# Performance work log

Measured on AMD Instinct MI355X. Metric: run time of the kernel, lower is better.

The kernel has to match this reference:

```python
import jax, jax.numpy as jnp
import numpy as np

TOP_K = 2          # n_activated_experts
ROUTE_SCALE = 1.0  # args.route_scale


def setup_inputs() -> dict:
    key = jax.random.key(0)
    ks = jax.random.split(key, 12)
    B, S, D, I, E = 8, 2048, 512, 1024, 8
    SH = 2 * I  # n_shared_experts * moe_inter_dim
    std = 0.02
    return {
        "x": jax.random.normal(ks[0], (B, S, D), jnp.float32),
        "gate_w": (jax.random.normal(ks[1], (E, D), jnp.float32) * std),
        "w1": (jax.random.normal(ks[2], (E, D, I), jnp.float32) * std),
        "w2": (jax.random.normal(ks[3], (E, I, D), jnp.float32) * std),
        "w3": (jax.random.normal(ks[4], (E, D, I), jnp.float32) * std),
        "sw1": (jax.random.normal(ks[5], (D, SH), jnp.float32) * std),
        "sb1": jnp.zeros((SH,), jnp.float32),
        "sw2": (jax.random.normal(ks[6], (SH, D), jnp.float32) * std),
        "sb2": jnp.zeros((D,), jnp.float32),
        "sw3": (jax.random.normal(ks[7], (D, SH), jnp.float32) * std),
        "sb3": jnp.zeros((SH,), jnp.float32),
    }


def reference(x, gate_w, w1, w2, w3, sw1, sb1, sw2, sb2, sw3, sb3):
    B, S, D = x.shape
    xt = x.reshape(-1, D)              # [T, D] tokens
    T = xt.shape[0]
    E = gate_w.shape[0]

    # --- Gate: sigmoid scores, top-k, renormalized weights ---
    scores = jax.nn.sigmoid(xt @ gate_w.T)                 # [T, E]
    topv, topi = jax.lax.top_k(scores, TOP_K)              # [T, K]
    wts = topv / jnp.sum(topv, axis=-1, keepdims=True)
    wts = wts * ROUTE_SCALE

    # Dense combine weights: zero for non-selected experts -> faithful to
    # the torch masked scatter-accumulate over the expert loop.
    cw = jnp.zeros((T, E), xt.dtype).at[jnp.arange(T)[:, None], topi].add(wts)

    # --- Routed SwiGLU experts (ffn_bias=False) ---
    y = jnp.zeros_like(xt)
    for e in range(E):  # fixed small structural loop over experts
        h = jax.nn.silu(xt @ w1[e]) * (xt @ w3[e])         # [T, I]
        y = y + cw[:, e:e + 1] * (h @ w2[e])               # combine

    # --- Load-balance aux loss L_ExpBal ---
    counts = jnp.zeros((E,), xt.dtype).at[topi.reshape(-1)].add(1.0)
    f_i = E * counts / (TOP_K * T)
    P_i = cw.sum(axis=0) / T   # per-expert sum of routed weights
    L_ExpBal = jnp.sum(f_i * P_i)

    # --- Shared experts MLP (biased Linear, SwiGLU) ---
    z = (jax.nn.silu(xt @ sw1 + sb1) * (xt @ sw3 + sb3)) @ sw2 + sb2

    return (y + z).reshape(B, S, D), L_ExpBal
```

## Files before the change

### kernel.cpp

```cpp
#include <hip/hip_runtime.h>
#include <math.h>
#include <stdint.h>

#define T_TOK 16384
#define DDIM  512
#define IDIM  1024
#define NEXP  8
#define SHDIM 2048
#define MT_R  264
#define MPAD  (MT_R * 128)
#define GBLK  256

typedef unsigned short u16;
typedef short bf16x8 __attribute__((ext_vector_type(8)));
typedef float f32x4 __attribute__((ext_vector_type(4)));

__device__ __forceinline__ u16 f2bf(float f) {
    unsigned u = __float_as_uint(f);
    u += 0x7FFF + ((u >> 16) & 1);
    return (u16)(u >> 16);
}
__device__ __forceinline__ float bf2f(u16 h) {
    return __uint_as_float((unsigned)h << 16);
}

__device__ __forceinline__ void gload_lds16(const void* g, void* l) {
    __builtin_amdgcn_global_load_lds(
        (const __attribute__((address_space(1))) void*)g,
        (__attribute__((address_space(3))) void*)l, 16, 0, 0);
}

__device__ __forceinline__ int xcd_swz(int id, int nwg) {
    return (id & 7) * (nwg >> 3) + (id >> 3);
}

__device__ __forceinline__ int ksw(int r) { return (r & 3) ^ ((r >> 2) & 3); }

__global__ void k_zero(int* cursors) {
    int i = threadIdx.x;
    if (i < NEXP) cursors[i] = 0;
}

__global__ __launch_bounds__(256) void k_gate(
    const float* __restrict__ x, const float* __restrict__ gw,
    int* __restrict__ topi, float* __restrict__ wts,
    int* __restrict__ pcnt, float* __restrict__ pps, u16* __restrict__ xb)
{
    __shared__ int   cnt[NEXP];
    __shared__ float ps[NEXP];
    const int tid = threadIdx.x;
    if (tid < NEXP) { cnt[tid] = 0; ps[tid] = 0.f; }
    __syncthreads();
    const int wid = tid >> 6, lane = tid & 63;

    const float4* gw4 = (const float4*)gw;
    float4 g0[NEXP], g1[NEXP];
#pragma unroll
    for (int e = 0; e < NEXP; e++) {
        g0[e] = gw4[e * 128 + lane];
        g1[e] = gw4[e * 128 + 64 + lane];
    }

    const int t0 = blockIdx.x * 64 + wid * 16;
    for (int u = 0; u < 16; u++) {
        int t = t0 + u;
        const float4* xr4 = (const float4*)(x + (size_t)t * DDIM);
        float4 v0 = xr4[lane];
        float4 v1 = xr4[64 + lane];
        ushort4 o0 = { f2bf(v0.x), f2bf(v0.y), f2bf(v0.z), f2bf(v0.w) };
// ... 29 lines not shown
            atomicAdd(&cnt[i1], 1); atomicAdd(&cnt[i2], 1);
            atomicAdd(&ps[i1], wa); atomicAdd(&ps[i2], wb);
        }
    }
    __syncthreads();
    if (tid < NEXP) {
        pcnt[blockIdx.x * NEXP + tid] = cnt[tid];
        pps[blockIdx.x * NEXP + tid]  = ps[tid];
    }
}

__global__ void k_scan(const int* __restrict__ pcnt, const float* __restrict__ pps,
                       int* __restrict__ off_pad, float* __restrict__ out_loss)
{
    __shared__ int   scnt[8][NEXP];
    __shared__ float sps[8][NEXP];
    int tid = threadIdx.x;
    if (tid < 64) {
        int e = tid & 7, part = tid >> 3;
        int c = 0; float p = 0.f;
        for (int b = part * 32; b < part * 32 + 32; b++) {
            c += pcnt[b * NEXP + e];
            p += pps[b * NEXP + e];
        }
        scnt[part][e] = c; sps[part][e] = p;
    }
    __syncthreads();
    if (tid == 0) {
        int off = 0; float L = 0.f;
        for (int e = 0; e < NEXP; e++) {
            int c = 0; float p = 0.f;
            for (int q = 0; q < 8; q++) { c += scnt[q][e]; p += sps[q][e]; }
            off_pad[e] = off;
            off += (c + 127) & ~127;
            float f = (float)NEXP * (float)c / (float)(2 * T_TOK);
            L += f * (p / (float)T_TOK);
        }
        off_pad[NEXP] = off;
        out_loss[0] = L;
    }
}

__global__ void k_fillperm(int* __restrict__ perm, u16* __restrict__ zpad) {
    int i = blockIdx.x * blockDim.x + threadIdx.x;
    if (i < MPAD) perm[i] = -1;
    if (blockIdx.x == 0 && threadIdx.x < 256) ((unsigned*)zpad)[threadIdx.x] = 0u;
}

__global__ __launch_bounds__(256) void k_scatter(
    const int* __restrict__ topi, const float* __restrict__ wts,
    const int* __restrict__ off_pad, int* __restrict__ cursors,
    int* __restrict__ perm, float* __restrict__ pw, int* __restrict__ inv)
{
    __shared__ int lcnt[NEXP];
    __shared__ int lbase[NEXP];
    int tid = threadIdx.x;
    if (tid < NEXP) lcnt[tid] = 0;
    __syncthreads();
    int t = blockIdx.x * 256 + tid;
    int e0 = topi[2 * t], e1 = topi[2 * t + 1];
    int p0 = atomicAdd(&lcnt[e0], 1);
    int p1 = atomicAdd(&lcnt[e1], 1);
    __syncthreads();
    if (tid < NEXP) lbase[tid] = atomicAdd(&cursors[tid], lcnt[tid]);
    __syncthreads();
    int s0 = off_pad[e0] + lbase[e0] + p0;
    int s1 = off_pad[e1] + lbase[e1] + p1;
    perm[s0] = t; pw[s0] = wts[2 * t];
    perm[s1] = t; pw[s1] = wts[2 * t + 1];
    inv[2 * t] = s0; inv[2 * t + 1] = s1;
}

__global__ __launch_bounds__(256) void k_transpose(const float* __restrict__ src,
                                                   u16* __restrict__ dst, int R, int C)
{
    __shared__ u16 t[64][68];
    const float* s = src + (size_t)blockIdx.z * R * C;
    u16* d = dst + (size_t)blockIdx.z * R * C;
    int r0 = blockIdx.y * 64, c0 = blockIdx.x * 64;
    int tid = threadIdx.x;
    int lr = tid >> 4, lc = (tid & 15) * 4;
#pragma unroll
    for (int u = 0; u < 4; u++) {
        int r = lr + u * 16;
        float4 v = *(const float4*)&s[(size_t)(r0 + r) * C + c0 + lc];
        t[lc + 0][r] = f2bf(v.x);
        t[lc + 1][r] = f2bf(v.y);
        t[lc + 2][r] = f2bf(v.z);
        t[lc + 3][r] = f2bf(v.w);
    }
    __syncthreads();
    int wr = tid >> 4, wc = (tid & 15) * 4;
#pragma unroll
    for (int u = 0; u < 4; u++) {
        int c = wr + u * 16;
        ushort4 o = { t[c][wc], t[c][wc + 1], t[c][wc + 2], t[c][wc + 3] };
        *(ushort4*)&d[(size_t)(c0 + c) * R + r0 + wc] = o;
    }
}

template<bool ROUTED, bool BIAS>
__global__ __launch_bounds__(256, 2) void k_s1(
    const u16* __restrict__ Axb, const u16* __restrict__ B1t, const u16* __restrict__ B3t,
    const float* __restrict__ bias1, const float* __restrict__ bias3,
    u16* __restrict__ H, int ldh, const int* __restrict__ off_pad,
    const int* __restrict__ perm, const u16* __restrict__ zpad)
{
    __shared__ __align__(16) unsigned char smem[3 * 24576];
    const int nwg = gridDim.x * gridDim.y;
    const int id  = xcd_swz(blockIdx.y * gridDim.x + blockIdx.x, nwg);
    const int m0 = (id / gridDim.x) * 128;
    const int n0 = (id % gridDim.x) * 128;
    if (ROUTED && m0 >= off_pad[NEXP]) return;
    const u16* b1 = B1t; const u16* b3 = B3t;
    if (ROUTED) {
        int e = 0;
        while (off_pad[e + 1] <= m0) e++;
        b1 += (size_t)e * IDIM * DDIM;
        b3 += (size_t)e * IDIM * DDIM;
    }
    const int tid = threadIdx.x;
    const int wid = tid >> 6, lane = tid & 63;
    const int fr = lane & 15, hi = lane >> 4;
    const int wrow = (wid >> 1) * 64, wcol = (wid & 1) * 64;

    const u16* ap[2]; const u16* b1p[2]; const u16* b3p[2];
    int dst_[2];
#pragma unroll
    for (int s = 0; s < 2; s++) {
        int r = s * 64 + (tid >> 2);
        int goff = ((tid & 3) ^ ksw(r)) * 8;
        dst_[s] = s * 4096 + tid * 16;
        if (ROUTED) {
            int tok = perm[m0 + r];
            ap[s] = (tok >= 0 ? Axb + (size_t)tok * DDIM : zpad) + goff;
        } else {
            ap[s] = Axb + (size_t)(m0 + r) * DDIM + goff;
        }
        b1p[s] = b1 + (size_t)(n0 + r) * DDIM + goff;
        b3p[s] = b3 + (size_t)(n0 + r) * DDIM + goff;
    }
    int aoff[4], boff[4];
#pragma unroll
    for (int i = 0; i < 4; i++) {
        int ar = wrow + i * 16 + fr;
        aoff[i] = ar * 64 + ((hi ^ ksw(ar)) << 4);
        int br = wcol + i * 16 + fr;
        boff[i] = br * 64 + ((hi ^ ksw(br)) << 4);
    }

    f32x4 acc1[4][4], acc3[4][4];
#pragma unroll
    for (int i = 0; i < 4; i++)
#pragma unroll
        for (int j = 0; j < 4; j++) { acc1[i][j] = {0.f, 0.f, 0.f, 0.f}; acc3[i][j] = {0.f, 0.f, 0.f, 0.f}; }

    const int NT = DDIM / 32;
#pragma unroll
    for (int t = 0; t < 2; t++) {
        unsigned char* bb = smem + t * 24576;
#pragma unroll
        for (int s = 0; s < 2; s++) {
            gload_lds16(ap[s]  + t * 32, bb + dst_[s]);
            gload_lds16(b1p[s] + t * 32, bb + 8192  + dst_[s]);
            gload_lds16(b3p[s] + t * 32, bb + 16384 + dst_[s]);
        }
    }

    int bufc = 0;
    for (int t = 0; t < NT; t++) {
        int bufn = bufc + 2; if (bufn >= 3) bufn -= 3;
        if (t + 2 < NT) {
            unsigned char* bb = smem + bufn * 24576;
            int k2 = (t + 2) * 32;
#pragma unroll
            for (int s = 0; s < 2; s++) {
                gload_lds16(ap[s]  + k2, bb + dst_[s]);
                gload_lds16(b1p[s] + k2, bb + 8192  + dst_[s]);
                gload_lds16(b3p[s] + k2, bb + 16384 + dst_[s]);
            }
            asm volatile("s_waitcnt vmcnt(12)" ::: "memory");
        } else if (t + 2 == NT) {
            asm volatile("s_waitcnt vmcnt(6)" ::: "memory");
        } else {
            asm volatile("s_waitcnt vmcnt(0)" ::: "memory");
        }
        __builtin_amdgcn_s_barrier();
        __builtin_amdgcn_sched_barrier(0);
        const unsigned char* cb = smem + bufc * 24576;
        bf16x8 av[4], b1v[4], b3v[4];
#pragma unroll
        for (int i = 0; i < 4; i++) {
            av[i]  = *(const bf16x8*)(cb + aoff[i]);
            b1v[i] = *(const bf16x8*)(cb + 8192  + boff[i]);
            b3v[i] = *(const bf16x8*)(cb + 16384 + boff[i]);
        }
        __builtin_amdgcn_s_setprio(1);
#pragma unroll
        for (int i = 0; i < 4; i++)
#pragma unroll
            for (int j = 0; j < 4; j++) {
                acc1[i][j] = __builtin_amdgcn_mfma_f32_16x16x32_bf16(av[i], b1v[j], acc1[i][j], 0, 0, 0);
                acc3[i][j] = __builtin_amdgcn_mfma_f32_16x16x32_bf16(av[i], b3v[j], acc3[i][j], 0, 0, 0);
            }
        __builtin_amdgcn_s_setprio(0);
        __builtin_amdgcn_sched_barrier(0);
        __builtin_amdgcn_s_barrier();
        bufc++; if (bufc >= 3) bufc -= 3;
    }

    const int rr = hi * 4;
#pragma unroll
    for (int i = 0; i < 4; i++) {
#pragma unroll
        for (int j = 0; j < 4; j++) {
            int col = n0 + wcol + j * 16 + fr;
            float bb1 = BIAS ? bias1[col] : 0.f;
            float bb3 = BIAS ? bias3[col] : 0.f;
#pragma unroll
            for (int r = 0; r < 4; r++) {
                int row = m0 + wrow + i * 16 + rr + r;
                float v1 = acc1[i][j][r] + bb1;
                float v3 = acc3[i][j][r] + bb3;
                float hv = (v1 / (1.f + __expf(-v1))) * v3;
                H[(size_t)row * ldh + col] = f2bf(hv);
            }
        }
    }
}

template<int K, bool ROUTED>
__global__ __launch_bounds__(256, 3) void k_s2(
    const u16* __restrict__ A, const u16* __restrict__ Bt,
    const float* __restrict__ bias2, float* __restrict__ out,
    u16* __restrict__ ytmp, const int* __restrict__ off_pad)
{
    __shared__ __align__(16) unsigned char smem[3 * 16384];
    const int nwg = gridDim.x * gridDim.y;
    const int id  = xcd_swz(blockIdx.y * gridDim.x + blockIdx.x, nwg);
    const int m0 = (id / gridDim.x) * 128;
    const int n0 = (id % gridDim.x) * 128;
    if (ROUTED && m0 >= off_pad[NEXP]) return;
    const u16* bt = Bt;
    if (ROUTED) {
        int e = 0;
        while (off_pad[e + 1] <= m0) e++;
        bt += (size_t)e * DDIM * IDIM;
    }
    const int tid = threadIdx.x;
    const int wid = tid >> 6, lane = tid & 63;
    const int fr = lane & 15, hi = lane >> 4;
    const int wrow = (wid >> 1) * 64, wcol = (wid & 1) * 64;

    const u16* ap[2]; const u16* bp[2];
    int dst_[2];
#pragma unroll
    for (int s = 0; s < 2; s++) {
        int r = s * 64 + (tid >> 2);
        int goff = ((tid & 3) ^ ksw(r)) * 8;
        dst_[s] = s * 4096 + tid * 16;
        ap[s] = A  + (size_t)(m0 + r) * K + goff;
        bp[s] = bt + (size_t)(n0 + r) * K + goff;
    }
    int aoff[4], boff[4];
#pragma unroll
    for (int i = 0; i < 4; i++) {
        int ar = wrow + i * 16 + fr;
        aoff[i] = ar * 64 + ((hi ^ ksw(ar)) << 4);
        int br = wcol + i * 16 + fr;
        boff[i] = br * 64 + ((hi ^ ksw(br)) << 4);
    }

    f32x4 acc[4][4];
#pragma unroll
    for (int i = 0; i < 4; i++)
#pragma unroll
        for (int j = 0; j < 4; j++) acc[i][j] = {0.f, 0.f, 0.f, 0.f};

    const int NT = K / 32;
#pragma unroll
    for (int t = 0; t < 2; t++) {
        unsigned char* bb = smem + t * 16384;
#pragma unroll
        for (int s = 0; s < 2; s++) {
            gload_lds16(ap[s] + t * 32, bb + dst_[s]);
            gload_lds16(bp[s] + t * 32, bb + 8192 + dst_[s]);
        }
    }

    int bufc = 0;
    for (int t = 0; t < NT; t++) {
        int bufn = bufc + 2; if (bufn >= 3) bufn -= 3;
        if (t + 2 < NT) {
            unsigned char* bb = smem + bufn * 16384;
            int k2 = (t + 2) * 32;
#pragma unroll
            for (int s = 0; s < 2; s++) {
                gload_lds16(ap[s] + k2, bb + dst_[s]);
                gload_lds16(bp[s] + k2, bb + 8192 + dst_[s]);
            }
            asm volatile("s_waitcnt vmcnt(8)" ::: "memory");
        } else if (t + 2 == NT) {
            asm volatile("s_waitcnt vmcnt(4)" ::: "memory");
        } else {
            asm volatile("s_waitcnt vmcnt(0)" ::: "memory");
        }
        __builtin_amdgcn_s_barrier();
        __builtin_amdgcn_sched_barrier(0);
        const unsigned char* cb = smem + bufc * 16384;
        bf16x8 av[4], bv[4];
#pragma unroll
        for (int i = 0; i < 4; i++) {
            av[i] = *(const bf16x8*)(cb + aoff[i]);
            bv[i] = *(const bf16x8*)(cb + 8192 + boff[i]);
        }
        __builtin_amdgcn_s_setprio(1);
#pragma unroll
        for (int i = 0; i < 4; i++)
#pragma unroll
            for (int j = 0; j < 4; j++)
                acc[i][j] = __builtin_amdgcn_mfma_f32_16x16x32_bf16(av[i], bv[j], acc[i][j], 0, 0, 0);
        __builtin_amdgcn_s_setprio(0);
        __builtin_amdgcn_sched_barrier(0);
        __builtin_amdgcn_s_barrier();
        bufc++; if (bufc >= 3) bufc -= 3;
    }

    const int rr = hi * 4;
#pragma unroll
    for (int i = 0; i < 4; i++) {
#pragma unroll
        for (int r = 0; r < 4; r++) {
            int row = m0 + wrow + i * 16 + rr + r;
#pragma unroll
            for (int j = 0; j < 4; j++) {
                int col = n0 + wcol + j * 16 + fr;
                float v = acc[i][j][r];
                if (ROUTED) {
                    ytmp[(size_t)row * DDIM + col] = f2bf(v);
                } else {
                    out[(size_t)row * DDIM + col] = v + bias2[col];
                }
            }
        }
    }
}

__global__ __launch_bounds__(256) void k_combine(
    const u16* __restrict__ ytmp, const int* __restrict__ inv,
    const float* __restrict__ wts, float* __restrict__ out)
{
    int idx = blockIdx.x * 256 + threadIdx.x;
    int t = idx >> 7;
    int c = (idx & 127) * 4;
    int s0 = inv[2 * t], s1 = inv[2 * t + 1];
    float w0 = wts[2 * t], w1 = wts[2 * t + 1];
    ushort4 a = *(const ushort4*)&ytmp[(size_t)s0 * DDIM + c];
    ushort4 b = *(const ushort4*)&ytmp[(size_t)s1 * DDIM + c];
    float4 o = *(float4*)&out[(size_t)t * DDIM + c];
    o.x += w0 * bf2f(a.x) + w1 * bf2f(b.x);
    o.y += w0 * bf2f(a.y) + w1 * bf2f(b.y);
    o.z += w0 * bf2f(a.z) + w1 * bf2f(b.z);
    o.w += w0 * bf2f(a.w) + w1 * bf2f(b.w);
    *(float4*)&out[(size_t)t * DDIM + c] = o;
}

extern "C" void kernel_launch(void* const* d_in, const int* in_sizes, int n_in,
                              void* d_out, int out_size, void* d_ws, size_t ws_size,
                              hipStream_t stream)
{
    const float* x   = (const float*)d_in[0];
    const float* gw  = (const float*)d_in[1];
    const float* w1  = (const float*)d_in[2];
    const float* w2  = (const float*)d_in[3];
    const float* w3  = (const float*)d_in[4];
    const float* sw1 = (const float*)d_in[5];
    const float* sb1 = (const float*)d_in[6];
    const float* sw2 = (const float*)d_in[7];
    const float* sb2 = (const float*)d_in[8];
    const float* sw3 = (const float*)d_in[9];
    const float* sb3 = (const float*)d_in[10];
    float* out = (float*)d_out;

    char* ws = (char*)d_ws;
    size_t off = 0;
    int*   topi    = (int*)(ws + off);   off += (size_t)2 * T_TOK * 4;
    float* wts     = (float*)(ws + off); off += (size_t)2 * T_TOK * 4;
    int*   perm    = (int*)(ws + off);   off += (size_t)MPAD * 4;
    float* pw      = (float*)(ws + off); off += (size_t)MPAD * 4;
    int*   cursors = (int*)(ws + off);   off += 256;
    int*   off_pad = (int*)(ws + off);   off += 256;
    int*   pcnt    = (int*)(ws + off);   off += (size_t)GBLK * NEXP * 4;
    float* pps     = (float*)(ws + off); off += (size_t)GBLK * NEXP * 4;
    int*   inv     = (int*)(ws + off);   off += (size_t)2 * T_TOK * 4;
    u16*   zpad    = (u16*)(ws + off);   off += 1024;
    u16*   xb      = (u16*)(ws + off);   off += (size_t)T_TOK * DDIM * 2;
    u16*   ytmp    = (u16*)(ws + off);   off += (size_t)MPAD * DDIM * 2;
    u16*   w1T     = (u16*)(ws + off);   off += (size_t)NEXP * IDIM * DDIM * 2;
    u16*   w3T     = (u16*)(ws + off);   off += (size_t)NEXP * IDIM * DDIM * 2;
    u16*   w2T     = (u16*)(ws + off);   off += (size_t)NEXP * DDIM * IDIM * 2;
    u16*   sw1T    = (u16*)(ws + off);   off += (size_t)SHDIM * DDIM * 2;
    u16*   sw3T    = (u16*)(ws + off);   off += (size_t)SHDIM * DDIM * 2;
    u16*   sw2T    = (u16*)(ws + off);   off += (size_t)DDIM * SHDIM * 2;
    u16*   hb      = (u16*)(ws + off);   off += (size_t)MPAD * IDIM * 2;

    k_zero<<<1, 64, 0, stream>>>(cursors);
    k_gate<<<GBLK, 256, 0, stream>>>(x, gw, topi, wts, pcnt, pps, xb);
    k_scan<<<1, 64, 0, stream>>>(pcnt, pps, off_pad, out + (size_t)T_TOK * DDIM);
    k_fillperm<<<MPAD / 256, 256, 0, stream>>>(perm, zpad);
    k_scatter<<<T_TOK / 256, 256, 0, stream>>>(topi, wts, off_pad, cursors, perm, pw, inv);

    k_transpose<<<dim3(IDIM / 64, DDIM / 64, NEXP), 256, 0, stream>>>(w1, w1T, DDIM, IDIM);
    k_transpose<<<dim3(IDIM / 64, DDIM / 64, NEXP), 256, 0, stream>>>(w3, w3T, DDIM, IDIM);
    k_transpose<<<dim3(DDIM / 64, IDIM / 64, NEXP), 256, 0, stream>>>(w2, w2T, IDIM, DDIM);
    k_transpose<<<dim3(SHDIM / 64, DDIM / 64, 1), 256, 0, stream>>>(sw1, sw1T, DDIM, SHDIM);
    k_transpose<<<dim3(SHDIM / 64, DDIM / 64, 1), 256, 0, stream>>>(sw3, sw3T, DDIM, SHDIM);
    k_transpose<<<dim3(DDIM / 64, SHDIM / 64, 1), 256, 0, stream>>>(sw2, sw2T, SHDIM, DDIM);

    k_s1<false, true><<<dim3(SHDIM / 128, T_TOK / 128), 256, 0, stream>>>(
        xb, sw1T, sw3T, sb1, sb3, hb, SHDIM, nullptr, nullptr, nullptr);
    k_s2<SHDIM, false><<<dim3(DDIM / 128, T_TOK / 128), 256, 0, stream>>>(
        hb, sw2T, sb2, out, nullptr, nullptr);
    k_s1<true, false><<<dim3(IDIM / 128, MT_R), 256, 0, stream>>>(
        xb, w1T, w3T, nullptr, nullptr, hb, IDIM, off_pad, perm, zpad);
    k_s2<IDIM, true><<<dim3(DDIM / 128, MT_R), 256, 0, stream>>>(
        hb, w2T, nullptr, nullptr, ytmp, off_pad);
    k_combine<<<(T_TOK * DDIM / 4) / 256, 256, 0, stream>>>(ytmp, inv, wts, out);
}
```

Measured before the change: 354.0 us.

## Fuse w1/w3 into interleaved weight and use 256x256 tiles in up-projection GEMM

The w1 and w3 weights are transposed into one interleaved matrix, with 128-row blocks of w1 and w3 alternating, so the first-stage GEMM loads a single B operand. The up-projection kernel moves to 512 threads with 256x256 output tiles and splits each k-step into two MFMA phases, interleaving A and B loads between them. The w3 accumulators are exchanged through LDS for the SwiGLU epilogue. Routed expert padding grows to multiples of 256, which adds padded rows, and LDS use per block rises to 96KB, which may limit occupancy.

```diff
diff --git a/kernel.cpp b/kernel.cpp
--- a/kernel.cpp
+++ b/kernel.cpp
@@ -7,8 +7,7 @@
 #define IDIM  1024
 #define NEXP  8
 #define SHDIM 2048
-#define MT_R  264
-#define MPAD  (MT_R * 128)
+#define MPAD  34816
 #define GBLK  256
 
 typedef unsigned short u16;
@@ -33,8 +32,6 @@
 __device__ __forceinline__ int xcd_swz(int id, int nwg) {
     return (id & 7) * (nwg >> 3) + (id >> 3);
 }
-
-__device__ __forceinline__ int ksw(int r) { return (r & 3) ^ ((r >> 2) & 3); }
 
 __global__ void k_zero(int* cursors) {
     int i = threadIdx.x;
@@ -130,7 +127,7 @@
             int c = 0; float p = 0.f;
             for (int q = 0; q < 8; q++) { c += scnt[q][e]; p += sps[q][e]; }
             off_pad[e] = off;
-            off += (c + 127) & ~127;
+            off += (c + 255) & ~255;
             float f = (float)NEXP * (float)c / (float)(2 * T_TOK);
             L += f * (p / (float)T_TOK);
         }
@@ -170,11 +167,12 @@
 }
 
 __global__ __launch_bounds__(256) void k_transpose(const float* __restrict__ src,
-                                                   u16* __restrict__ dst, int R, int C)
+                                                   u16* __restrict__ dst, int R, int C,
+                                                   int rmul, int radd, int zrows)
 {
     __shared__ u16 t[64][68];
     const float* s = src + (size_t)blockIdx.z * R * C;
-    u16* d = dst + (size_t)blockIdx.z * R * C;
+    u16* d = dst + (size_t)blockIdx.z * zrows * R;
     int r0 = blockIdx.y * 64, c0 = blockIdx.x * 64;
     int tid = threadIdx.x;
     int lr = tid >> 4, lc = (tid & 15) * 4;
@@ -192,140 +190,187 @@
 #pragma unroll
     for (int u = 0; u < 4; u++) {
         int c = wr + u * 16;
+        int gc = c0 + c;
+        int rp = (gc >> 7) * rmul + (gc & 127) + radd;
         ushort4 o = { t[c][wc], t[c][wc + 1], t[c][wc + 2], t[c][wc + 3] };
-        *(ushort4*)&d[(size_t)(c0 + c) * R + r0 + wc] = o;
+        *(ushort4*)&d[(size_t)rp * R + r0 + wc] = o;
     }
 }
 
 template<bool ROUTED, bool BIAS>
-__global__ __launch_bounds__(256, 2) void k_s1(
-    const u16* __restrict__ Axb, const u16* __restrict__ B1t, const u16* __restrict__ B3t,
+__global__ __launch_bounds__(512, 2) void k_s1(
+    const u16* __restrict__ Axb, const u16* __restrict__ Bt,
     const float* __restrict__ bias1, const float* __restrict__ bias3,
     u16* __restrict__ H, int ldh, const int* __restrict__ off_pad,
     const int* __restrict__ perm, const u16* __restrict__ zpad)
 {
-    __shared__ __align__(16) unsigned char smem[3 * 24576];
+    __shared__ __align__(16) unsigned char smem[3 * 32768];
     const int nwg = gridDim.x * gridDim.y;
     const int id  = xcd_swz(blockIdx.y * gridDim.x + blockIdx.x, nwg);
-    const int m0 = (id / gridDim.x) * 128;
-    const int n0 = (id % gridDim.x) * 128;
+    const int mt = id / gridDim.x, nt = id % gridDim.x;
+    const int m0 = mt * 256;
     if (ROUTED && m0 >= off_pad[NEXP]) return;
-    const u16* b1 = B1t; const u16* b3 = B3t;
+    const u16* B = Bt;
     if (ROUTED) {
         int e = 0;
         while (off_pad[e + 1] <= m0) e++;
-        b1 += (size_t)e * IDIM * DDIM;
-        b3 += (size_t)e * IDIM * DDIM;
-    }
+        B += (size_t)e * (2 * IDIM) * DDIM;
+    }
+    const int n0r = nt * 256;
+
     const int tid = threadIdx.x;
     const int wid = tid >> 6, lane = tid & 63;
+    const int wm = wid >> 2, wn = wid & 3;
     const int fr = lane & 15, hi = lane >> 4;
-    const int wrow = (wid >> 1) * 64, wcol = (wid & 1) * 64;
-
-    const u16* ap[2]; const u16* b1p[2]; const u16* b3p[2];
-    int dst_[2];
-#pragma unroll
-    for (int s = 0; s < 2; s++) {
-        int r = s * 64 + (tid >> 2);
-        int goff = ((tid & 3) ^ ksw(r)) * 8;
-        dst_[s] = s * 4096 + tid * 16;
+
+    const int r128 = tid >> 2;
+    const int ksw2 = (r128 >> 1) & 3;
+    const int goff = ((tid & 3) ^ ksw2) * 8;
+    const u16* asrc[2]; const u16* bsrc[2];
+#pragma unroll
+    for (int h = 0; h < 2; h++) {
         if (ROUTED) {
-            int tok = perm[m0 + r];
-            ap[s] = (tok >= 0 ? Axb + (size_t)tok * DDIM : zpad) + goff;
+            int tok = perm[m0 + h * 128 + r128];
+            asrc[h] = (tok >= 0 ? Axb + (size_t)tok * DDIM : zpad) + goff;
         } else {
-            ap[s] = Axb + (size_t)(m0 + r) * DDIM + goff;
-        }
-        b1p[s] = b1 + (size_t)(n0 + r) * DDIM + goff;
-        b3p[s] = b3 + (size_t)(n0 + r) * DDIM + goff;
-    }
-    int aoff[4], boff[4];
-#pragma unroll
-    for (int i = 0; i < 4; i++) {
-        int ar = wrow + i * 16 + fr;
-        aoff[i] = ar * 64 + ((hi ^ ksw(ar)) << 4);
-        int br = wcol + i * 16 + fr;
-        boff[i] = br * 64 + ((hi ^ ksw(br)) << 4);
-    }
-
-    f32x4 acc1[4][4], acc3[4][4];
-#pragma unroll
-    for (int i = 0; i < 4; i++)
-#pragma unroll
-        for (int j = 0; j < 4; j++) { acc1[i][j] = {0.f, 0.f, 0.f, 0.f}; acc3[i][j] = {0.f, 0.f, 0.f, 0.f}; }
+            asrc[h] = Axb + (size_t)(m0 + h * 128 + r128) * DDIM + goff;
+        }
+        bsrc[h] = B + (size_t)(n0r + h * 128 + r128) * DDIM + goff;
+    }
+    const int dstb = tid * 16;
+
+    int aoff[8], boff[4];
+#pragma unroll
+    for (int i = 0; i < 8; i++) {
+        int ar = wm * 128 + i * 16 + fr;
+        aoff[i] = (ar >> 7) * 8192 + (ar & 127) * 64 + ((hi ^ ((ar >> 1) & 3)) << 4);
+    }
+#pragma unroll
+    for (int j = 0; j < 4; j++) {
+        int br = wn * 64 + j * 16 + fr;
+        boff[j] = 16384 + (br >> 7) * 8192 + (br & 127) * 64 + ((hi ^ ((br >> 1) & 3)) << 4);
+    }
+
+    f32x4 acc[8][4];
+#pragma unroll
+    for (int i = 0; i < 8; i++)
+#pragma unroll
+        for (int j = 0; j < 4; j++) acc[i][j] = {0.f, 0.f, 0.f, 0.f};
 
     const int NT = DDIM / 32;
 #pragma unroll
     for (int t = 0; t < 2; t++) {
-        unsigned char* bb = smem + t * 24576;
-#pragma unroll
-        for (int s = 0; s < 2; s++) {
-            gload_lds16(ap[s]  + t * 32, bb + dst_[s]);
-            gload_lds16(b1p[s] + t * 32, bb + 8192  + dst_[s]);
-            gload_lds16(b3p[s] + t * 32, bb + 16384 + dst_[s]);
-        }
-    }
+        unsigned char* bb = smem + t * 32768;
+#pragma unroll
+        for (int h = 0; h < 2; h++) {
+            gload_lds16(asrc[h] + t * 32, bb + h * 8192 + dstb);
+            gload_lds16(bsrc[h] + t * 32, bb + 16384 + h * 8192 + dstb);
+        }
+    }
+    asm volatile("s_waitcnt vmcnt(4)" ::: "memory");
+    __builtin_amdgcn_s_barrier();
 
     int bufc = 0;
     for (int t = 0; t < NT; t++) {
+        unsigned char* cb = smem + bufc * 32768;
         int bufn = bufc + 2; if (bufn >= 3) bufn -= 3;
+        unsigned char* nb = smem + bufn * 32768;
+        const int k2 = (t + 2) * 32;
+
+        bf16x8 bv[4], av0[4];
+#pragma unroll
+        for (int j = 0; j < 4; j++) bv[j] = *(const bf16x8*)(cb + boff[j]);
+#pragma unroll
+        for (int i = 0; i < 4; i++) av0[i] = *(const bf16x8*)(cb + aoff[i]);
         if (t + 2 < NT) {
-            unsigned char* bb = smem + bufn * 24576;
-            int k2 = (t + 2) * 32;
-#pragma unroll
-            for (int s = 0; s < 2; s++) {
-                gload_lds16(ap[s]  + k2, bb + dst_[s]);
-                gload_lds16(b1p[s] + k2, bb + 8192  + dst_[s]);
-                gload_lds16(b3p[s] + k2, bb + 16384 + dst_[s]);
-            }
-            asm volatile("s_waitcnt vmcnt(12)" ::: "memory");
-        } else if (t + 2 == NT) {
-            asm volatile("s_waitcnt vmcnt(6)" ::: "memory");
-        } else {
-            asm volatile("s_waitcnt vmcnt(0)" ::: "memory");
+            gload_lds16(asrc[0] + k2, nb + dstb);
+            gload_lds16(asrc[1] + k2, nb + 8192 + dstb);
         }
         __builtin_amdgcn_s_barrier();
+        asm volatile("s_waitcnt lgkmcnt(0)" ::: "memory");
         __builtin_amdgcn_sched_barrier(0);
-        const unsigned char* cb = smem + bufc * 24576;
-        bf16x8 av[4], b1v[4], b3v[4];
-#pragma unroll
-        for (int i = 0; i < 4; i++) {
-            av[i]  = *(const bf16x8*)(cb + aoff[i]);
-            b1v[i] = *(const bf16x8*)(cb + 8192  + boff[i]);
-            b3v[i] = *(const bf16x8*)(cb + 16384 + boff[i]);
-        }
         __builtin_amdgcn_s_setprio(1);
 #pragma unroll
         for (int i = 0; i < 4; i++)
 #pragma unroll
-            for (int j = 0; j < 4; j++) {
-                acc1[i][j] = __builtin_amdgcn_mfma_f32_16x16x32_bf16(av[i], b1v[j], acc1[i][j], 0, 0, 0);
-                acc3[i][j] = __builtin_amdgcn_mfma_f32_16x16x32_bf16(av[i], b3v[j], acc3[i][j], 0, 0, 0);
-            }
+            for (int j = 0; j < 4; j++)
+                acc[i][j] = __builtin_amdgcn_mfma_f32_16x16x32_bf16(av0[i], bv[j], acc[i][j], 0, 0, 0);
         __builtin_amdgcn_s_setprio(0);
         __builtin_amdgcn_sched_barrier(0);
         __builtin_amdgcn_s_barrier();
+
+        bf16x8 av1[4];
+#pragma unroll
+        for (int i = 0; i < 4; i++) av1[i] = *(const bf16x8*)(cb + aoff[4 + i]);
+        if (t + 2 < NT) {
+            gload_lds16(bsrc[0] + k2, nb + 16384 + dstb);
+            gload_lds16(bsrc[1] + k2, nb + 16384 + 8192 + dstb);
+            asm volatile("s_waitcnt vmcnt(4)" ::: "memory");
+        } else if (t + 2 == NT) {
+            asm volatile("s_waitcnt vmcnt(0)" ::: "memory");
+        }
+        __builtin_amdgcn_s_barrier();
+        asm volatile("s_waitcnt lgkmcnt(0)" ::: "memory");
+        __builtin_amdgcn_sched_barrier(0);
+        __builtin_amdgcn_s_setprio(1);
+#pragma unroll
+        for (int i = 0; i < 4; i++)
+#pragma unroll
+            for (int j = 0; j < 4; j++)
+                acc[4 + i][j] = __builtin_amdgcn_mfma_f32_16x16x32_bf16(av1[i], bv[j], acc[4 + i][j], 0, 0, 0);
+        __builtin_amdgcn_s_setprio(0);
+        __builtin_amdgcn_sched_barrier(0);
+        __builtin_amdgcn_s_barrier();
+
         bufc++; if (bufc >= 3) bufc -= 3;
     }
 
-    const int rr = hi * 4;
-#pragma unroll
-    for (int i = 0; i < 4; i++) {
-#pragma unroll
-        for (int j = 0; j < 4; j++) {
-            int col = n0 + wcol + j * 16 + fr;
-            float bb1 = BIAS ? bias1[col] : 0.f;
-            float bb3 = BIAS ? bias3[col] : 0.f;
-#pragma unroll
-            for (int r = 0; r < 4; r++) {
-                int row = m0 + wrow + i * 16 + rr + r;
-                float v1 = acc1[i][j][r] + bb1;
-                float v3 = acc3[i][j][r] + bb3;
-                float hv = (v1 / (1.f + __expf(-v1))) * v3;
-                H[(size_t)row * ldh + col] = f2bf(hv);
+    float* c3ex = (float*)smem;
+#pragma unroll
+    for (int half = 0; half < 2; half++) {
+        __syncthreads();
+        if (wn >= 2) {
+#pragma unroll
+            for (int q = 0; q < 4; q++) {
+                int i = half * 4 + q;
+#pragma unroll
+                for (int j = 0; j < 4; j++) {
+                    int col = (wn - 2) * 64 + j * 16 + fr;
+#pragma unroll
+                    for (int r = 0; r < 4; r++) {
+                        int brow = wm * 64 + q * 16 + hi * 4 + r;
+                        c3ex[brow * 128 + (col ^ ((brow & 1) << 4))] = acc[i][j][r];
+                    }
+                }
             }
         }
-    }
-}
+        __syncthreads();
+        if (wn < 2) {
+#pragma unroll
+            for (int q = 0; q < 4; q++) {
+                int i = half * 4 + q;
+#pragma unroll
+                for (int j = 0; j < 4; j++) {
+                    int colw = wn * 64 + j * 16 + fr;
+                    int gcol = nt * 128 + colw;
+                    float b1 = BIAS ? bias1[gcol] : 0.f;
+                    float b3 = BIAS ? bias3[gcol] : 0.f;
+#pragma unroll
+                    for (int r = 0; r < 4; r++) {
+                        int brow = wm * 64 + q * 16 + hi * 4 + r;
+                        int grow = m0 + wm * 128 + half * 64 + q * 16 + hi * 4 + r;
+                        float v1 = acc[i][j][r] + b1;
+                        float v3 = c3ex[brow * 128 + (colw ^ ((brow & 1) << 4))] + b3;
+                        float hv = (v1 / (1.f + __expf(-v1))) * v3;
+                        H[(size_t)grow * ldh + gcol] = f2bf(hv);
+                    }
+                }
+            }
+        }
+    }
+}
+
+__device__ __forceinline__ int ksw(int r) { return (r & 3) ^ ((r >> 2) & 3); }
 
 template<int K, bool ROUTED>
 __global__ __launch_bounds__(256, 3) void k_s2(
@@ -494,11 +539,9 @@
     u16*   zpad    = (u16*)(ws + off);   off += 1024;
     u16*   xb      = (u16*)(ws + off);   off += (size_t)T_TOK * DDIM * 2;
     u16*   ytmp    = (u16*)(ws + off);   off += (size_t)MPAD * DDIM * 2;
-    u16*   w1T     = (u16*)(ws + off);   off += (size_t)NEXP * IDIM * DDIM * 2;
-    u16*   w3T     = (u16*)(ws + off);   off += (size_t)NEXP * IDIM * DDIM * 2;
+    u16*   w13Ts   = (u16*)(ws + off);   off += (size_t)2 * SHDIM * DDIM * 2;
+    u16*   w13Tr   = (u16*)(ws + off);   off += (size_t)NEXP * 2 * IDIM * DDIM * 2;
     u16*   w2T     = (u16*)(ws + off);   off += (size_t)NEXP * DDIM * IDIM * 2;
-    u16*   sw1T    = (u16*)(ws + off);   off += (size_t)SHDIM * DDIM * 2;
-    u16*   sw3T    = (u16*)(ws + off);   off += (size_t)SHDIM * DDIM * 2;
     u16*   sw2T    = (u16*)(ws + off);   off += (size_t)DDIM * SHDIM * 2;
     u16*   hb      = (u16*)(ws + off);   off += (size_t)MPAD * IDIM * 2;
 
@@ -508,20 +551,20 @@
     k_fillperm<<<MPAD / 256, 256, 0, stream>>>(perm, zpad);
     k_scatter<<<T_TOK / 256, 256, 0, stream>>>(topi, wts, off_pad, cursors, perm, pw, inv);
 
-    k_transpose<<<dim3(IDIM / 64, DDIM / 64, NEXP), 256, 0, stream>>>(w1, w1T, DDIM, IDIM);
-    k_transpose<<<dim3(IDIM / 64, DDIM / 64, NEXP), 256, 0, stream>>>(w3, w3T, DDIM, IDIM);
-    k_transpose<<<dim3(DDIM / 64, IDIM / 64, NEXP), 256, 0, stream>>>(w2, w2T, IDIM, DDIM);
-    k_transpose<<<dim3(SHDIM / 64, DDIM / 64, 1), 256, 0, stream>>>(sw1, sw1T, DDIM, SHDIM);
-    k_transpose<<<dim3(SHDIM / 64, DDIM / 64, 1), 256, 0, stream>>>(sw3, sw3T, DDIM, SHDIM);
-    k_transpose<<<dim3(DDIM / 64, SHDIM / 64, 1), 256, 0, stream>>>(sw2, sw2T, SHDIM, DDIM);
-
-    k_s1<false, true><<<dim3(SHDIM / 128, T_TOK / 128), 256, 0, stream>>>(
-        xb, sw1T, sw3T, sb1, sb3, hb, SHDIM, nullptr, nullptr, nullptr);
+    k_transpose<<<dim3(SHDIM / 64, DDIM / 64, 1), 256, 0, stream>>>(sw1, w13Ts, DDIM, SHDIM, 256, 0,   2 * SHDIM);
+    k_transpose<<<dim3(SHDIM / 64, DDIM / 64, 1), 256, 0, stream>>>(sw3, w13Ts, DDIM, SHDIM, 256, 128, 2 * SHDIM);
+    k_transpose<<<dim3(IDIM / 64, DDIM / 64, NEXP), 256, 0, stream>>>(w1, w13Tr, DDIM, IDIM, 256, 0,   2 * IDIM);
+    k_transpose<<<dim3(IDIM / 64, DDIM / 64, NEXP), 256, 0, stream>>>(w3, w13Tr, DDIM, IDIM, 256, 128, 2 * IDIM);
+    k_transpose<<<dim3(DDIM / 64, IDIM / 64, NEXP), 256, 0, stream>>>(w2, w2T, IDIM, DDIM, 128, 0, DDIM);
+    k_transpose<<<dim3(DDIM / 64, SHDIM / 64, 1), 256, 0, stream>>>(sw2, sw2T, SHDIM, DDIM, 128, 0, DDIM);
+
+    k_s1<false, true><<<dim3(16, T_TOK / 256), 512, 0, stream>>>(
+        xb, w13Ts, sb1, sb3, hb, SHDIM, nullptr, nullptr, nullptr);
     k_s2<SHDIM, false><<<dim3(DDIM / 128, T_TOK / 128), 256, 0, stream>>>(
         hb, sw2T, sb2, out, nullptr, nullptr);
-    k_s1<true, false><<<dim3(IDIM / 128, MT_R), 256, 0, stream>>>(
-        xb, w1T, w3T, nullptr, nullptr, hb, IDIM, off_pad, perm, zpad);
-    k_s2<IDIM, true><<<dim3(DDIM / 128, MT_R), 256, 0, stream>>>(
+    k_s1<true, false><<<dim3(8, MPAD / 256), 512, 0, stream>>>(
+        xb, w13Tr, nullptr, nullptr, hb, IDIM, off_pad, perm, zpad);
+    k_s2<IDIM, true><<<dim3(DDIM / 128, MPAD / 128), 256, 0, stream>>>(
         hb, w2T, nullptr, nullptr, ytmp, off_pad);
     k_combine<<<(T_TOK * DDIM / 4) / 256, 256, 0, stream>>>(ytmp, inv, wts, out);
 }
```

Result: slower. 415.8 us (+17.5%).

## Use 256-row GEMM tiles with interleaved w1/w3 weights and XCD-aware block mapping

Applied to the files above, without the earlier changes.

Each GEMM tile grows from 128x128 to 256 rows, with every wave owning a 64x128 output slab. The w1 and w3 weights are transposed into one interleaved buffer in 64-row chunks, so the SwiGLU stage loads a single B tile and finds the gate and up halves side by side. Expert padding is raised to multiples of 256 to match the new M tile. A per-kernel block-to-tile mapping replaces the generic XCD swizzle so that tiles sharing A rows land on the same XCD for L2 reuse. Larger tiles increase arithmetic intensity but use more registers and LDS per block, and fewer blocks run per CU.

```diff
diff --git a/kernel.cpp b/kernel.cpp
--- a/kernel.cpp
+++ b/kernel.cpp
@@ -7,8 +7,7 @@
 #define IDIM  1024
 #define NEXP  8
 #define SHDIM 2048
-#define MT_R  264
-#define MPAD  (MT_R * 128)
+#define MPAD  34816
 #define GBLK  256
 
 typedef unsigned short u16;
@@ -28,10 +27,6 @@
     __builtin_amdgcn_global_load_lds(
         (const __attribute__((address_space(1))) void*)g,
         (__attribute__((address_space(3))) void*)l, 16, 0, 0);
-}
-
-__device__ __forceinline__ int xcd_swz(int id, int nwg) {
-    return (id & 7) * (nwg >> 3) + (id >> 3);
 }
 
 __device__ __forceinline__ int ksw(int r) { return (r & 3) ^ ((r >> 2) & 3); }
@@ -130,7 +125,7 @@
             int c = 0; float p = 0.f;
             for (int q = 0; q < 8; q++) { c += scnt[q][e]; p += sps[q][e]; }
             off_pad[e] = off;
-            off += (c + 127) & ~127;
+            off += (c + 255) & ~255;
             float f = (float)NEXP * (float)c / (float)(2 * T_TOK);
             L += f * (p / (float)T_TOK);
         }
@@ -170,11 +165,12 @@
 }
 
 __global__ __launch_bounds__(256) void k_transpose(const float* __restrict__ src,
-                                                   u16* __restrict__ dst, int R, int C)
+                                                   u16* __restrict__ dst, int R, int C,
+                                                   int rmul, int radd, int zrows)
 {
     __shared__ u16 t[64][68];
     const float* s = src + (size_t)blockIdx.z * R * C;
-    u16* d = dst + (size_t)blockIdx.z * R * C;
+    u16* d = dst + (size_t)blockIdx.z * zrows * R;
     int r0 = blockIdx.y * 64, c0 = blockIdx.x * 64;
     int tid = threadIdx.x;
     int lr = tid >> 4, lc = (tid & 15) * 4;
@@ -192,77 +188,107 @@
 #pragma unroll
     for (int u = 0; u < 4; u++) {
         int c = wr + u * 16;
+        int gc = c0 + c;
+        int rp = (gc >> 6) * rmul + (gc & 63) + radd;
         ushort4 o = { t[c][wc], t[c][wc + 1], t[c][wc + 2], t[c][wc + 3] };
-        *(ushort4*)&d[(size_t)(c0 + c) * R + r0 + wc] = o;
-    }
-}
-
-template<bool ROUTED, bool BIAS>
+        *(ushort4*)&d[(size_t)rp * R + r0 + wc] = o;
+    }
+}
+
+template<int MODE>
+__device__ __forceinline__ void blockmap(int id, int& mt, int& nt) {
+    if (MODE == 0) {
+        int xcd = id >> 8, p = id & 255;
+        int sm = p >> 7, r = p & 127;
+        mt = xcd * 8 + sm * 4 + (r & 3);
+        nt = r >> 2;
+    } else if (MODE == 1) {
+        int xcd = id / 272, p = id % 272;
+        mt = xcd * 17 + p / 16;
+        nt = p % 16;
+    } else if (MODE == 2) {
+        int xcd = id >> 5, p = id & 31;
+        mt = xcd * 8 + (p >> 2);
+        nt = p & 3;
+    } else {
+        int xcd = id / 68, p = id % 68;
+        mt = xcd * 17 + (p >> 2);
+        nt = p & 3;
+    }
+}
+
+template<int MODE, bool ROUTED, bool BIAS>
 __global__ __launch_bounds__(256, 2) void k_s1(
-    const u16* __restrict__ Axb, const u16* __restrict__ B1t, const u16* __restrict__ B3t,
+    const u16* __restrict__ Axb, const u16* __restrict__ Bt,
     const float* __restrict__ bias1, const float* __restrict__ bias3,
     u16* __restrict__ H, int ldh, const int* __restrict__ off_pad,
     const int* __restrict__ perm, const u16* __restrict__ zpad)
 {
     __shared__ __align__(16) unsigned char smem[3 * 24576];
-    const int nwg = gridDim.x * gridDim.y;
-    const int id  = xcd_swz(blockIdx.y * gridDim.x + blockIdx.x, nwg);
-    const int m0 = (id / gridDim.x) * 128;
-    const int n0 = (id % gridDim.x) * 128;
+    int mt, nt;
+    blockmap<MODE>(blockIdx.y * gridDim.x + blockIdx.x, mt, nt);
+    const int m0 = mt * 256;
     if (ROUTED && m0 >= off_pad[NEXP]) return;
-    const u16* b1 = B1t; const u16* b3 = B3t;
+    const u16* B = Bt;
     if (ROUTED) {
         int e = 0;
         while (off_pad[e + 1] <= m0) e++;
-        b1 += (size_t)e * IDIM * DDIM;
-        b3 += (size_t)e * IDIM * DDIM;
-    }
+        B += (size_t)e * (2 * IDIM) * DDIM;
+    }
+    const int n0r = nt * 128;
+
     const int tid = threadIdx.x;
-    const int wid = tid >> 6, lane = tid & 63;
+    const int wm = tid >> 6, lane = tid & 63;
     const int fr = lane & 15, hi = lane >> 4;
-    const int wrow = (wid >> 1) * 64, wcol = (wid & 1) * 64;
-
-    const u16* ap[2]; const u16* b1p[2]; const u16* b3p[2];
-    int dst_[2];
-#pragma unroll
-    for (int s = 0; s < 2; s++) {
-        int r = s * 64 + (tid >> 2);
-        int goff = ((tid & 3) ^ ksw(r)) * 8;
-        dst_[s] = s * 4096 + tid * 16;
+
+    const u16* asrc[4]; const u16* bsrc[2];
+    const int grow = tid >> 2;
+    const int gsl  = tid & 3;
+#pragma unroll
+    for (int s = 0; s < 4; s++) {
+        int r = s * 64 + grow;
+        int goff = (gsl ^ ksw(r)) * 8;
         if (ROUTED) {
             int tok = perm[m0 + r];
-            ap[s] = (tok >= 0 ? Axb + (size_t)tok * DDIM : zpad) + goff;
+            asrc[s] = (tok >= 0 ? Axb + (size_t)tok * DDIM : zpad) + goff;
         } else {
-            ap[s] = Axb + (size_t)(m0 + r) * DDIM + goff;
-        }
-        b1p[s] = b1 + (size_t)(n0 + r) * DDIM + goff;
-        b3p[s] = b3 + (size_t)(n0 + r) * DDIM + goff;
-    }
-    int aoff[4], boff[4];
+            asrc[s] = Axb + (size_t)(m0 + r) * DDIM + goff;
+        }
+    }
+#pragma unroll
+    for (int s = 0; s < 2; s++) {
+        int r = s * 64 + grow;
+        int goff = (gsl ^ ksw(r)) * 8;
+        bsrc[s] = B + (size_t)(n0r + r) * DDIM + goff;
+    }
+    const int dstT = tid * 16;
+
+    int aoff[4], boff[8];
 #pragma unroll
     for (int i = 0; i < 4; i++) {
-        int ar = wrow + i * 16 + fr;
+        int ar = wm * 64 + i * 16 + fr;
         aoff[i] = ar * 64 + ((hi ^ ksw(ar)) << 4);
-        int br = wcol + i * 16 + fr;
-        boff[i] = br * 64 + ((hi ^ ksw(br)) << 4);
-    }
-
-    f32x4 acc1[4][4], acc3[4][4];
+    }
+#pragma unroll
+    for (int j = 0; j < 8; j++) {
+        int br = j * 16 + fr;
+        boff[j] = 16384 + br * 64 + ((hi ^ ksw(br)) << 4);
+    }
+
+    f32x4 acc[4][8];
 #pragma unroll
     for (int i = 0; i < 4; i++)
 #pragma unroll
-        for (int j = 0; j < 4; j++) { acc1[i][j] = {0.f, 0.f, 0.f, 0.f}; acc3[i][j] = {0.f, 0.f, 0.f, 0.f}; }
+        for (int j = 0; j < 8; j++) acc[i][j] = {0.f, 0.f, 0.f, 0.f};
 
     const int NT = DDIM / 32;
 #pragma unroll
     for (int t = 0; t < 2; t++) {
         unsigned char* bb = smem + t * 24576;
 #pragma unroll
-        for (int s = 0; s < 2; s++) {
-            gload_lds16(ap[s]  + t * 32, bb + dst_[s]);
-            gload_lds16(b1p[s] + t * 32, bb + 8192  + dst_[s]);
-            gload_lds16(b3p[s] + t * 32, bb + 16384 + dst_[s]);
-        }
+        for (int s = 0; s < 4; s++) gload_lds16(asrc[s] + t * 32, bb + s * 4096 + dstT);
+#pragma unroll
+        for (int s = 0; s < 2; s++) gload_lds16(bsrc[s] + t * 32, bb + 16384 + s * 4096 + dstT);
     }
 
     int bufc = 0;
@@ -272,11 +298,9 @@
             unsigned char* bb = smem + bufn * 24576;
             int k2 = (t + 2) * 32;
 #pragma unroll
-            for (int s = 0; s < 2; s++) {
-                gload_lds16(ap[s]  + k2, bb + dst_[s]);
-                gload_lds16(b1p[s] + k2, bb + 8192  + dst_[s]);
-                gload_lds16(b3p[s] + k2, bb + 16384 + dst_[s]);
-            }
+            for (int s = 0; s < 4; s++) gload_lds16(asrc[s] + k2, bb + s * 4096 + dstT);
+#pragma unroll
+            for (int s = 0; s < 2; s++) gload_lds16(bsrc[s] + k2, bb + 16384 + s * 4096 + dstT);
             asm volatile("s_waitcnt vmcnt(12)" ::: "memory");
         } else if (t + 2 == NT) {
             asm volatile("s_waitcnt vmcnt(6)" ::: "memory");
@@ -286,58 +310,53 @@
         __builtin_amdgcn_s_barrier();
         __builtin_amdgcn_sched_barrier(0);
         const unsigned char* cb = smem + bufc * 24576;
-        bf16x8 av[4], b1v[4], b3v[4];
-#pragma unroll
-        for (int i = 0; i < 4; i++) {
-            av[i]  = *(const bf16x8*)(cb + aoff[i]);
-            b1v[i] = *(const bf16x8*)(cb + 8192  + boff[i]);
-            b3v[i] = *(const bf16x8*)(cb + 16384 + boff[i]);
-        }
+        bf16x8 av[4], bv[8];
+#pragma unroll
+        for (int i = 0; i < 4; i++) av[i] = *(const bf16x8*)(cb + aoff[i]);
+#pragma unroll
+        for (int j = 0; j < 8; j++) bv[j] = *(const bf16x8*)(cb + boff[j]);
         __builtin_amdgcn_s_setprio(1);
 #pragma unroll
         for (int i = 0; i < 4; i++)
 #pragma unroll
-            for (int j = 0; j < 4; j++) {
-                acc1[i][j] = __builtin_amdgcn_mfma_f32_16x16x32_bf16(av[i], b1v[j], acc1[i][j], 0, 0, 0);
-                acc3[i][j] = __builtin_amdgcn_mfma_f32_16x16x32_bf16(av[i], b3v[j], acc3[i][j], 0, 0, 0);
-            }
+            for (int j = 0; j < 8; j++)
+                acc[i][j] = __builtin_amdgcn_mfma_f32_16x16x32_bf16(av[i], bv[j], acc[i][j], 0, 0, 0);
         __builtin_amdgcn_s_setprio(0);
         __builtin_amdgcn_sched_barrier(0);
         __builtin_amdgcn_s_barrier();
         bufc++; if (bufc >= 3) bufc -= 3;
     }
 
-    const int rr = hi * 4;
 #pragma unroll
     for (int i = 0; i < 4; i++) {
 #pragma unroll
         for (int j = 0; j < 4; j++) {
-            int col = n0 + wcol + j * 16 + fr;
-            float bb1 = BIAS ? bias1[col] : 0.f;
-            float bb3 = BIAS ? bias3[col] : 0.f;
+            int hcol = nt * 64 + j * 16 + fr;
+            float b1 = BIAS ? bias1[hcol] : 0.f;
+            float b3 = BIAS ? bias3[hcol] : 0.f;
 #pragma unroll
             for (int r = 0; r < 4; r++) {
-                int row = m0 + wrow + i * 16 + rr + r;
-                float v1 = acc1[i][j][r] + bb1;
-                float v3 = acc3[i][j][r] + bb3;
+                int row = m0 + wm * 64 + i * 16 + hi * 4 + r;
+                float v1 = acc[i][j][r] + b1;
+                float v3 = acc[i][j + 4][r] + b3;
                 float hv = (v1 / (1.f + __expf(-v1))) * v3;
-                H[(size_t)row * ldh + col] = f2bf(hv);
+                H[(size_t)row * ldh + hcol] = f2bf(hv);
             }
         }
     }
 }
 
-template<int K, bool ROUTED>
-__global__ __launch_bounds__(256, 3) void k_s2(
+template<int K, int MODE, bool ROUTED>
+__global__ __launch_bounds__(256, 2) void k_s2(
     const u16* __restrict__ A, const u16* __restrict__ Bt,
     const float* __restrict__ bias2, float* __restrict__ out,
     u16* __restrict__ ytmp, const int* __restrict__ off_pad)
 {
-    __shared__ __align__(16) unsigned char smem[3 * 16384];
-    const int nwg = gridDim.x * gridDim.y;
-    const int id  = xcd_swz(blockIdx.y * gridDim.x + blockIdx.x, nwg);
-    const int m0 = (id / gridDim.x) * 128;
-    const int n0 = (id % gridDim.x) * 128;
+    __shared__ __align__(16) unsigned char smem[3 * 24576];
+    int mt, nt;
+    blockmap<MODE>(blockIdx.y * gridDim.x + blockIdx.x, mt, nt);
+    const int m0 = mt * 256;
+    const int n0 = nt * 128;
     if (ROUTED && m0 >= off_pad[NEXP]) return;
     const u16* bt = Bt;
     if (ROUTED) {
@@ -346,77 +365,81 @@
         bt += (size_t)e * DDIM * IDIM;
     }
     const int tid = threadIdx.x;
-    const int wid = tid >> 6, lane = tid & 63;
+    const int wm = tid >> 6, lane = tid & 63;
     const int fr = lane & 15, hi = lane >> 4;
-    const int wrow = (wid >> 1) * 64, wcol = (wid & 1) * 64;
-
-    const u16* ap[2]; const u16* bp[2];
-    int dst_[2];
+
+    const u16* asrc[4]; const u16* bsrc[2];
+    const int grow = tid >> 2;
+    const int gsl  = tid & 3;
+#pragma unroll
+    for (int s = 0; s < 4; s++) {
+        int r = s * 64 + grow;
+        asrc[s] = A + (size_t)(m0 + r) * K + (gsl ^ ksw(r)) * 8;
+    }
 #pragma unroll
     for (int s = 0; s < 2; s++) {
-        int r = s * 64 + (tid >> 2);
-        int goff = ((tid & 3) ^ ksw(r)) * 8;
-        dst_[s] = s * 4096 + tid * 16;
-        ap[s] = A  + (size_t)(m0 + r) * K + goff;
-        bp[s] = bt + (size_t)(n0 + r) * K + goff;
-    }
-    int aoff[4], boff[4];
+        int r = s * 64 + grow;
+        bsrc[s] = bt + (size_t)(n0 + r) * K + (gsl ^ ksw(r)) * 8;
+    }
+    const int dstT = tid * 16;
+
+    int aoff[4], boff[8];
 #pragma unroll
     for (int i = 0; i < 4; i++) {
-        int ar = wrow + i * 16 + fr;
+        int ar = wm * 64 + i * 16 + fr;
         aoff[i] = ar * 64 + ((hi ^ ksw(ar)) << 4);
-        int br = wcol + i * 16 + fr;
-        boff[i] = br * 64 + ((hi ^ ksw(br)) << 4);
-    }
-
-    f32x4 acc[4][4];
+    }
+#pragma unroll
+    for (int j = 0; j < 8; j++) {
+        int br = j * 16 + fr;
+        boff[j] = 16384 + br * 64 + ((hi ^ ksw(br)) << 4);
+    }
+
+    f32x4 acc[4][8];
 #pragma unroll
     for (int i = 0; i < 4; i++)
 #pragma unroll
-        for (int j = 0; j < 4; j++) acc[i][j] = {0.f, 0.f, 0.f, 0.f};
+        for (int j = 0; j < 8; j++) acc[i][j] = {0.f, 0.f, 0.f, 0.f};
 
     const int NT = K / 32;
 #pragma unroll
     for (int t = 0; t < 2; t++) {
-        unsigned char* bb = smem + t * 16384;
-#pragma unroll
-        for (int s = 0; s < 2; s++) {
-            gload_lds16(ap[s] + t * 32, bb + dst_[s]);
-            gload_lds16(bp[s] + t * 32, bb + 8192 + dst_[s]);
-        }
+        unsigned char* bb = smem + t * 24576;
+#pragma unroll
+        for (int s = 0; s < 4; s++) gload_lds16(asrc[s] + t * 32, bb + s * 4096 + dstT);
+#pragma unroll
+        for (int s = 0; s < 2; s++) gload_lds16(bsrc[s] + t * 32, bb + 16384 + s * 4096 + dstT);
     }
 
     int bufc = 0;
     for (int t = 0; t < NT; t++) {
         int bufn = bufc + 2; if (bufn >= 3) bufn -= 3;
         if (t + 2 < NT) {
-            unsigned char* bb = smem + bufn * 16384;
+            unsigned char* bb = smem + bufn * 24576;
             int k2 = (t + 2) * 32;
 #pragma unroll
-            for (int s = 0; s < 2; s++) {
-                gload_lds16(ap[s] + k2, bb + dst_[s]);
-                gload_lds16(bp[s] + k2, bb + 8192 + dst_[s]);
-            }
-            asm volatile("s_waitcnt vmcnt(8)" ::: "memory");
+            for (int s = 0; s < 4; s++) gload_lds16(asrc[s] + k2, bb + s * 4096 + dstT);
+#pragma unroll
+            for (int s = 0; s < 2; s++) gload_lds16(bsrc[s] + k2, bb + 16384 + s * 4096 + dstT);
+            asm volatile("s_waitcnt vmcnt(12)" ::: "memory");
         } else if (t + 2 == NT) {
-            asm volatile("s_waitcnt vmcnt(4)" ::: "memory");
+            asm volatile("s_waitcnt vmcnt(6)" ::: "memory");
         } else {
             asm volatile("s_waitcnt vmcnt(0)" ::: "memory");
         }
         __builtin_amdgcn_s_barrier();
         __builtin_amdgcn_sched_barrier(0);
-        const unsigned char* cb = smem + bufc * 16384;
-        bf16x8 av[4], bv[4];
-#pragma unroll
-        for (int i = 0; i < 4; i++) {
-            av[i] = *(const bf16x8*)(cb + aoff[i]);
-            bv[i] = *(const bf16x8*)(cb + 8192 + boff[i]);
-        }
+        const unsigned char* cb = smem + bufc * 24576;
+        bf16x8 av[4], bv[8];
+#pragma unroll
+        for (int i = 0; i < 4; i++) av[i] = *(const bf16x8*)(cb + aoff[i]);
+#pragma unroll
+        for (int j = 0; j < 8; j++) bv[j] = *(const bf16x8*)(cb + boff[j]);
         __builtin_amdgcn_s_setprio(1);
 #pragma unroll
         for (int i = 0; i < 4; i++)
 #pragma unroll
-            for (int j = 0; j < 4; j++)
+            for (int j = 0; j < 8; j++)
                 acc[i][j] = __builtin_amdgcn_mfma_f32_16x16x32_bf16(av[i], bv[j], acc[i][j], 0, 0, 0);
         __builtin_amdgcn_s_setprio(0);
         __builtin_amdgcn_sched_barrier(0);
@@ -424,15 +447,14 @@
         bufc++; if (bufc >= 3) bufc -= 3;
     }
 
-    const int rr = hi * 4;
 #pragma unroll
     for (int i = 0; i < 4; i++) {
 #pragma unroll
         for (int r = 0; r < 4; r++) {
-            int row = m0 + wrow + i * 16 + rr + r;
-#pragma unroll
-            for (int j = 0; j < 4; j++) {
-                int col = n0 + wcol + j * 16 + fr;
+            int row = m0 + wm * 64 + i * 16 + hi * 4 + r;
+#pragma unroll
+            for (int j = 0; j < 8; j++) {
+                int col = n0 + j * 16 + fr;
                 float v = acc[i][j][r];
                 if (ROUTED) {
                     ytmp[(size_t)row * DDIM + col] = f2bf(v);
@@ -494,11 +516,9 @@
     u16*   zpad    = (u16*)(ws + off);   off += 1024;
     u16*   xb      = (u16*)(ws + off);   off += (size_t)T_TOK * DDIM * 2;
     u16*   ytmp    = (u16*)(ws + off);   off += (size_t)MPAD * DDIM * 2;
-    u16*   w1T     = (u16*)(ws + off);   off += (size_t)NEXP * IDIM * DDIM * 2;
-    u16*   w3T     = (u16*)(ws + off);   off += (size_t)NEXP * IDIM * DDIM * 2;
+    u16*   w13Ts   = (u16*)(ws + off);   off += (size_t)2 * SHDIM * DDIM * 2;
+    u16*   w13Tr   = (u16*)(ws + off);   off += (size_t)NEXP * 2 * IDIM * DDIM * 2;
     u16*   w2T     = (u16*)(ws + off);   off += (size_t)NEXP * DDIM * IDIM * 2;
-    u16*   sw1T    = (u16*)(ws + off);   off += (size_t)SHDIM * DDIM * 2;
-    u16*   sw3T    = (u16*)(ws + off);   off += (size_t)SHDIM * DDIM * 2;
     u16*   sw2T    = (u16*)(ws + off);   off += (size_t)DDIM * SHDIM * 2;
     u16*   hb      = (u16*)(ws + off);   off += (size_t)MPAD * IDIM * 2;
 
@@ -508,20 +528,20 @@
     k_fillperm<<<MPAD / 256, 256, 0, stream>>>(perm, zpad);
     k_scatter<<<T_TOK / 256, 256, 0, stream>>>(topi, wts, off_pad, cursors, perm, pw, inv);
 
-    k_transpose<<<dim3(IDIM / 64, DDIM / 64, NEXP), 256, 0, stream>>>(w1, w1T, DDIM, IDIM);
-    k_transpose<<<dim3(IDIM / 64, DDIM / 64, NEXP), 256, 0, stream>>>(w3, w3T, DDIM, IDIM);
-    k_transpose<<<dim3(DDIM / 64, IDIM / 64, NEXP), 256, 0, stream>>>(w2, w2T, IDIM, DDIM);
-    k_transpose<<<dim3(SHDIM / 64, DDIM / 64, 1), 256, 0, stream>>>(sw1, sw1T, DDIM, SHDIM);
-    k_transpose<<<dim3(SHDIM / 64, DDIM / 64, 1), 256, 0, stream>>>(sw3, sw3T, DDIM, SHDIM);
-    k_transpose<<<dim3(DDIM / 64, SHDIM / 64, 1), 256, 0, stream>>>(sw2, sw2T, SHDIM, DDIM);
-
-    k_s1<false, true><<<dim3(SHDIM / 128, T_TOK / 128), 256, 0, stream>>>(
-        xb, sw1T, sw3T, sb1, sb3, hb, SHDIM, nullptr, nullptr, nullptr);
-    k_s2<SHDIM, false><<<dim3(DDIM / 128, T_TOK / 128), 256, 0, stream>>>(
+    k_transpose<<<dim3(SHDIM / 64, DDIM / 64, 1), 256, 0, stream>>>(sw1, w13Ts, DDIM, SHDIM, 128, 0,  2 * SHDIM);
+    k_transpose<<<dim3(SHDIM / 64, DDIM / 64, 1), 256, 0, stream>>>(sw3, w13Ts, DDIM, SHDIM, 128, 64, 2 * SHDIM);
+    k_transpose<<<dim3(IDIM / 64, DDIM / 64, NEXP), 256, 0, stream>>>(w1, w13Tr, DDIM, IDIM, 128, 0,  2 * IDIM);
+    k_transpose<<<dim3(IDIM / 64, DDIM / 64, NEXP), 256, 0, stream>>>(w3, w13Tr, DDIM, IDIM, 128, 64, 2 * IDIM);
+    k_transpose<<<dim3(DDIM / 64, IDIM / 64, NEXP), 256, 0, stream>>>(w2, w2T, IDIM, DDIM, 64, 0, DDIM);
+    k_transpose<<<dim3(DDIM / 64, SHDIM / 64, 1), 256, 0, stream>>>(sw2, sw2T, SHDIM, DDIM, 64, 0, DDIM);
+
+    k_s1<0, false, true><<<dim3(32, 64), 256, 0, stream>>>(
+        xb, w13Ts, sb1, sb3, hb, SHDIM, nullptr, nullptr, nullptr);
+    k_s2<SHDIM, 2, false><<<dim3(4, 64), 256, 0, stream>>>(
         hb, sw2T, sb2, out, nullptr, nullptr);
-    k_s1<true, false><<<dim3(IDIM / 128, MT_R), 256, 0, stream>>>(
-        xb, w1T, w3T, nullptr, nullptr, hb, IDIM, off_pad, perm, zpad);
-    k_s2<IDIM, true><<<dim3(DDIM / 128, MT_R), 256, 0, stream>>>(
+    k_s1<1, true, false><<<dim3(16, 136), 256, 0, stream>>>(
+        xb, w13Tr, nullptr, nullptr, hb, IDIM, off_pad, perm, zpad);
+    k_s2<IDIM, 3, true><<<dim3(4, 136), 256, 0, stream>>>(
         hb, w2T, nullptr, nullptr, ytmp, off_pad);
     k_combine<<<(T_TOK * DDIM / 4) / 256, 256, 0, stream>>>(ytmp, inv, wts, out);
 }
```

Measured after the change: 376.5 us. +6.4%, slower.
